# Kernel tuning notes

Measured on AMD Instinct MI355X. Metric: run time of the kernel, lower is better.

Reference implementation:

```python
import jax, jax.numpy as jnp
import numpy as np

NEG_WEIGHT = 0.5   # args_config.lambda_
REG_WEIGHT = 1e-4  # args_config.l2 (dropout rate 0.0 -> identity)

N_USERS, N_ITEMS, DIM = 200000, 1000000, 64
BATCH, HIST = 4096, 200


def setup_inputs() -> dict:
    key = jax.random.key(0)
    k1, k2, k3, k4, k5 = jax.random.split(key, 5)
    users = jax.random.randint(k1, (BATCH,), 0, N_USERS, dtype=jnp.int64 if jax.config.jax_enable_x64 else jnp.int32).astype(jnp.int32)
    hist = jax.random.randint(k2, (N_USERS, HIST), 0, N_ITEMS).astype(jnp.int32)
    user_emb = jax.random.normal(k3, (N_USERS, DIM), dtype=jnp.float32) * 0.1
    item_emb = jax.random.normal(k4, (N_ITEMS, DIM), dtype=jnp.float32) * 0.1
    Hw = jax.random.normal(k5, (1, DIM), dtype=jnp.float32) * 0.1
    return {"users": users, "hist": hist, "user_emb": user_emb,
            "item_emb": item_emb, "Hw": Hw}


def reference(users, hist, user_emb, item_emb, Hw):
    h = Hw[0]                                   # [D]
    u = user_emb[users]                         # [B, D]
    items = item_emb[hist[users]]               # [B, L, D]
    # pos_score[b,l] = sum_d u[b,d] * items[b,l,d] * h[d]  (mul + H_i linear)
    pos_score = jnp.einsum('bd,bld,d->bl', u, items, h)
    # Gram matrices replace bmm(outer).sum(0): E^T E, U_b^T U_b, h h^T
    item_sum = item_emb.T @ item_emb            # [D, D]
    user_sum = u.T @ u                          # [D, D]
    H_sum = jnp.outer(h, h)                     # [D, D]
    t = jnp.sum(item_sum * user_sum * H_sum)
    loss = NEG_WEIGHT * t
    loss = loss + jnp.sum((1.0 - NEG_WEIGHT) * jnp.square(pos_score) - 2.0 * pos_score)
    # reg: 2-norm (Frobenius) of each full embedding table
    reg_loss = REG_WEIGHT * (jnp.linalg.norm(user_emb) + jnp.linalg.norm(item_emb))
    loss = loss + reg_loss
    return (loss, reg_loss, reg_loss)
```

## Files before the change

### kernel.cpp

```cpp
#include <hip/hip_runtime.h>
#include <hip/hip_bf16.h>

typedef __bf16 bf16x8 __attribute__((ext_vector_type(8)));
typedef float f32x16 __attribute__((ext_vector_type(16)));

template<bool GATHER>
static __device__ __forceinline__ void gram_body(
    const float* __restrict__ emb, const int* __restrict__ idx,
    int nrows, int nwaves_total, int blk,
    float* __restrict__ partial, float* __restrict__ red, int t) {
    const int lane = t & 63, wave = t >> 6;
    const int c = lane & 31, kh = lane >> 5;
    const int wid = blk * 4 + wave;
    const int step = nwaves_total * 16;

    f32x16 g00 = {}, g01 = {}, g11 = {};
    float cur0[8], cur1[8];

    int k0 = wid * 16;
    if (k0 < nrows) {
        const int kb = k0 + kh * 8;
#pragma unroll
        for (int j = 0; j < 8; ++j) {
            const size_t rb = (GATHER ? (size_t)idx[kb + j] : (size_t)(kb + j)) * 64;
            cur0[j] = emb[rb + c];
            cur1[j] = emb[rb + 32 + c];
        }
    }
    for (; k0 < nrows; k0 += step) {
        float nx0[8], nx1[8];
        const int k1 = k0 + step;
        if (k1 < nrows) {
            const int kb = k1 + kh * 8;
#pragma unroll
            for (int j = 0; j < 8; ++j) {
                const size_t rb = (GATHER ? (size_t)idx[kb + j] : (size_t)(kb + j)) * 64;
                nx0[j] = emb[rb + c];
                nx1[j] = emb[rb + 32 + c];
            }
        } else {
#pragma unroll
            for (int j = 0; j < 8; ++j) { nx0[j] = 0.f; nx1[j] = 0.f; }
        }
        bf16x8 f0, f1;
#pragma unroll
        for (int j = 0; j < 8; ++j) {
            f0[j] = (__bf16)cur0[j];
            f1[j] = (__bf16)cur1[j];
        }
        g00 = __builtin_amdgcn_mfma_f32_32x32x16_bf16(f0, f0, g00, 0, 0, 0);
        g01 = __builtin_amdgcn_mfma_f32_32x32x16_bf16(f0, f1, g01, 0, 0, 0);
        g11 = __builtin_amdgcn_mfma_f32_32x32x16_bf16(f1, f1, g11, 0, 0, 0);
#pragma unroll
        for (int j = 0; j < 8; ++j) { cur0[j] = nx0[j]; cur1[j] = nx1[j]; }
    }

    __syncthreads();
    for (int w = 0; w < 4; ++w) {
        if (wave == w) {
#pragma unroll
            for (int r = 0; r < 16; ++r) {
                const int cell = ((r & 3) + 8 * (r >> 2) + 4 * kh) * 32 + c;
                if (w == 0) {
                    red[cell] = g00[r]; red[1024 + cell] = g01[r]; red[2048 + cell] = g11[r];
                } else {
                    red[cell] += g00[r]; red[1024 + cell] += g01[r]; red[2048 + cell] += g11[r];
                }
            }
        }
        __syncthreads();
    }
    float* outp = partial + (size_t)blk * 3072;
    for (int i = t; i < 3072; i += 256) outp[i] = red[i];
}

__global__ __launch_bounds__(256) void gram_kernel(
    const float* __restrict__ emb, int nrows, int nwaves_total,
    float* __restrict__ partial) {
    __shared__ float red[3072];
    gram_body<false>(emb, nullptr, nrows, nwaves_total, blockIdx.x,
                     partial, red, threadIdx.x);
}

__global__ __launch_bounds__(256) void mix_kernel(
    const int* __restrict__ users, const int* __restrict__ hist,
    const float* __restrict__ user_emb, const float* __restrict__ item_emb,
    const float* __restrict__ Hw, int batch, int histL, int n_users,
    int NP, int NSS, int NU,
    float* __restrict__ p1, float* __restrict__ p2,
    float* __restrict__ pss, float* __restrict__ partB) {
    __shared__ float red[3072];
    const int bid = blockIdx.x, t = threadIdx.x;

    if (bid < NP) {
        const int lane = t & 63, wave = t >> 6;
        const int w = bid * 4 + wave;
        if (w >= batch) return;
        const int iu = users[w];
        const int k = lane & 15, g = lane >> 4;
        const float4 vu = *reinterpret_cast<const float4*>(user_emb + (size_t)iu * 64 + k * 4);
        const float4 vh = *reinterpret_cast<const float4*>(Hw + k * 4);
        const float4 uh = make_float4(vu.x * vh.x, vu.y * vh.y, vu.z * vh.z, vu.w * vh.w);
        const int* hrow = hist + (size_t)iu * histL;

        float s1 = 0.f, s2 = 0.f;
        int l = g;
        for (; l + 12 < histL; l += 16) {
            int it[4];
#pragma unroll
            for (int u = 0; u < 4; ++u) it[u] = hrow[l + 4 * u];
            float d[4];
#pragma unroll
            for (int u = 0; u < 4; ++u) {
                const float4 v = *reinterpret_cast<const float4*>(
                    item_emb + (size_t)it[u] * 64 + k * 4);
                d[u] = v.x * uh.x + v.y * uh.y + v.z * uh.z + v.w * uh.w;
            }
#pragma unroll
            for (int u = 0; u < 4; ++u) {
                float dd = d[u];
                dd += __shfl_xor(dd, 1, 16);
                dd += __shfl_xor(dd, 2, 16);
                dd += __shfl_xor(dd, 4, 16);
                dd += __shfl_xor(dd, 8, 16);
                s1 += dd;
                s2 = fmaf(dd, dd, s2);
            }
        }
        for (; l < histL; l += 4) {
            const int it = hrow[l];
            const float4 v = *reinterpret_cast<const float4*>(
                item_emb + (size_t)it * 64 + k * 4);
            float dd = v.x * uh.x + v.y * uh.y + v.z * uh.z + v.w * uh.w;
            dd += __shfl_xor(dd, 1, 16);
            dd += __shfl_xor(dd, 2, 16);
            dd += __shfl_xor(dd, 4, 16);
            dd += __shfl_xor(dd, 8, 16);
            s1 += dd;
            s2 = fmaf(dd, dd, s2);
        }
        s1 += __shfl_xor(s1, 16, 64); s1 += __shfl_xor(s1, 32, 64);
        s2 += __shfl_xor(s2, 16, 64); s2 += __shfl_xor(s2, 32, 64);
        if (lane == 0) { p1[w] = s1 * 0.0625f; p2[w] = s2 * 0.0625f; }
    } else if (bid < NP + NSS) {
        const int cid = bid - NP;
        const int n4 = n_users * 16;
        float s = 0.f;
        for (int i = cid * 256 + t; i < n4; i += NSS * 256) {
            const float4 v = reinterpret_cast<const float4*>(user_emb)[i];
            s = fmaf(v.x, v.x, s); s = fmaf(v.y, v.y, s);
            s = fmaf(v.z, v.z, s); s = fmaf(v.w, v.w, s);
        }
#pragma unroll
        for (int off = 32; off >= 1; off >>= 1) s += __shfl_xor(s, off, 64);
        if ((t & 63) == 0) red[t >> 6] = s;
        __syncthreads();
        if (t == 0) pss[cid] = red[0] + red[1] + red[2] + red[3];
    } else {
        gram_body<true>(user_emb, users, batch, NU * 4, bid - NP - NSS,
                        partB, red, t);
    }
}

__global__ __launch_bounds__(256) void reduce_gram_kernel(
    const float* __restrict__ pa, int na,
    const float* __restrict__ pb, int nb, float* __restrict__ part2) {
    const int bid = blockIdx.x;
    const int cellblk = bid % 24, seg = bid / 24;
    const int e = cellblk * 256 + threadIdx.x;
    const float* p; int n, ee;
    if (e < 3072) { p = pa; n = na; ee = e; }
    else          { p = pb; n = nb; ee = e - 3072; }
    const int chunk = (n + 7) >> 3;
    const int b0 = seg * chunk;
    int b1 = b0 + chunk; if (b1 > n) b1 = n;
    float s[4] = {0.f, 0.f, 0.f, 0.f};
    int b = b0;
    for (; b + 4 <= b1; b += 4)
#pragma unroll
        for (int u = 0; u < 4; ++u) s[u] += p[(size_t)(b + u) * 3072 + ee];
    for (; b < b1; ++b) s[0] += p[(size_t)b * 3072 + ee];
    part2[(size_t)seg * 6144 + e] = (s[0] + s[1]) + (s[2] + s[3]);
}

__global__ __launch_bounds__(1024) void finalize_kernel(
    const float* __restrict__ part2, const float* __restrict__ Hw,
    const float* __restrict__ p1, const float* __restrict__ p2, int npos,
    const float* __restrict__ pss, int nss, float* __restrict__ outp) {
    const int t = threadIdx.x;
    float tsum = 0.f, trace = 0.f, s1 = 0.f, s2 = 0.f, su = 0.f;
    for (int e = t; e < 3072; e += 1024) {
        float gi = 0.f, gu = 0.f;
#pragma unroll
        for (int seg = 0; seg < 8; ++seg) {
            gi += part2[(size_t)seg * 6144 + e];
            gu += part2[(size_t)seg * 6144 + 3072 + e];
        }
        const int tile = e >> 10, r = (e & 1023) >> 5, cc = e & 31;
        const int i = (tile == 2) ? r + 32 : r;
        const int j = (tile == 0) ? cc : cc + 32;
        const float w = (tile == 1) ? 2.0f : 1.0f;
        tsum += w * gi * gu * Hw[i] * Hw[j];
        if (i == j) trace += gi;
    }
    for (int e = t; e < npos; e += 1024) { s1 += p1[e]; s2 += p2[e]; }
    for (int e = t; e < nss; e += 1024) su += pss[e];
#pragma unroll
    for (int off = 32; off >= 1; off >>= 1) {
        tsum += __shfl_xor(tsum, off, 64);
        trace += __shfl_xor(trace, off, 64);
        s1 += __shfl_xor(s1, off, 64);
        s2 += __shfl_xor(s2, off, 64);
        su += __shfl_xor(su, off, 64);
    }
    __shared__ float rr[16][5];
    if ((t & 63) == 0) {
        const int w = t >> 6;
        rr[w][0] = tsum; rr[w][1] = trace; rr[w][2] = s1;
        rr[w][3] = s2;   rr[w][4] = su;
    }
    __syncthreads();
    if (t == 0) {
        float a[5] = {0.f, 0.f, 0.f, 0.f, 0.f};
        for (int w = 0; w < 16; ++w)
#pragma unroll
            for (int q = 0; q < 5; ++q) a[q] += rr[w][q];
        const float reg = 1e-4f * (sqrtf(a[4]) + sqrtf(a[1]));
        const float loss = 0.5f * a[0] + 0.5f * a[3] - 2.0f * a[2] + reg;
        outp[0] = loss; outp[1] = reg; outp[2] = reg;
    }
}

extern "C" void kernel_launch(void* const* d_in, const int* in_sizes, int n_in,
                              void* d_out, int out_size, void* d_ws, size_t ws_size,
                              hipStream_t stream) {
    const int*   users    = (const int*)d_in[0];
    const int*   hist     = (const int*)d_in[1];
    const float* user_emb = (const float*)d_in[2];
    const float* item_emb = (const float*)d_in[3];
    const float* Hw       = (const float*)d_in[4];
    float* outp = (float*)d_out;
    float* ws   = (float*)d_ws;

    const int n_users = in_sizes[2] / 64;
    const int n_items = in_sizes[3] / 64;
    const int batch   = in_sizes[0];
    const int histL   = in_sizes[1] / n_users;

    int NB_ITEM = 1024;
    const int NP  = (batch + 3) / 4;
    const int NSS = 512;
    const int NU  = 64;

    const size_t o_p1 = 0;
    const size_t o_p2 = o_p1 + (size_t)batch;
    const size_t o_ss = o_p2 + (size_t)batch;
    const size_t o_part2 = o_ss + NSS;
    const size_t o_part = o_part2 + 8 * 6144;
    long availf = (long)(ws_size / 4) - (long)o_part - (long)NU * 3072;
    if ((long)NB_ITEM * 3072 > availf) {
        NB_ITEM = (int)(availf / 3072);
        if (NB_ITEM < 8) NB_ITEM = 8;
    }
    float* partA = ws + o_part;
    float* partB = partA + (size_t)NB_ITEM * 3072;

    gram_kernel<<<NB_ITEM, 256, 0, stream>>>(
        item_emb, n_items, NB_ITEM * 4, partA);
    mix_kernel<<<NP + NSS + NU, 256, 0, stream>>>(
        users, hist, user_emb, item_emb, Hw, batch, histL, n_users,
        NP, NSS, NU, ws + o_p1, ws + o_p2, ws + o_ss, partB);
    reduce_gram_kernel<<<24 * 8, 256, 0, stream>>>(
        partA, NB_ITEM, partB, NU, ws + o_part2);
    finalize_kernel<<<1, 1024, 0, stream>>>(
        ws + o_part2, Hw, ws + o_p1, ws + o_p2, batch,
        ws + o_ss, NSS, outp);
}
```

Before: 111.7 us.

## Fuse item Gram kernel into mixed kernel and rebalance block counts

Merges the separate item-embedding Gram kernel into the mixed kernel, so the item Gram, the positive-score gather, the user sum-of-squares and the user Gram all run as block ranges of one launch and can overlap on the GPU. The positive-score section becomes a grid-stride loop over users with a fixed 512 blocks, and the block counts are retuned (768 item-Gram blocks, 192 sum-of-squares blocks, launch bounds with 6 blocks per CU). This removes one launch and the tail gap between the first two kernels, at the cost of coarser load balance and possible register pressure from the new launch bound.

```diff
diff --git a/kernel.cpp b/kernel.cpp
--- a/kernel.cpp
+++ b/kernel.cpp
@@ -74,51 +74,60 @@
     for (int i = t; i < 3072; i += 256) outp[i] = red[i];
 }
 
-__global__ __launch_bounds__(256) void gram_kernel(
-    const float* __restrict__ emb, int nrows, int nwaves_total,
-    float* __restrict__ partial) {
-    __shared__ float red[3072];
-    gram_body<false>(emb, nullptr, nrows, nwaves_total, blockIdx.x,
-                     partial, red, threadIdx.x);
-}
-
-__global__ __launch_bounds__(256) void mix_kernel(
+__global__ __launch_bounds__(256, 6) void fused_kernel(
     const int* __restrict__ users, const int* __restrict__ hist,
     const float* __restrict__ user_emb, const float* __restrict__ item_emb,
-    const float* __restrict__ Hw, int batch, int histL, int n_users,
-    int NP, int NSS, int NU,
-    float* __restrict__ p1, float* __restrict__ p2,
-    float* __restrict__ pss, float* __restrict__ partB) {
+    const float* __restrict__ Hw,
+    int n_users, int n_items, int batch, int histL,
+    int NA, int NP, int NSS, int NU,
+    float* __restrict__ partA, float* __restrict__ partB,
+    float* __restrict__ p1, float* __restrict__ p2, float* __restrict__ pss) {
     __shared__ float red[3072];
     const int bid = blockIdx.x, t = threadIdx.x;
 
-    if (bid < NP) {
+    if (bid < NA) {
+        gram_body<false>(item_emb, nullptr, n_items, NA * 4, bid,
+                         partA, red, t);
+    } else if (bid < NA + NP) {
+        const int pid = bid - NA;
         const int lane = t & 63, wave = t >> 6;
-        const int w = bid * 4 + wave;
-        if (w >= batch) return;
-        const int iu = users[w];
         const int k = lane & 15, g = lane >> 4;
-        const float4 vu = *reinterpret_cast<const float4*>(user_emb + (size_t)iu * 64 + k * 4);
-        const float4 vh = *reinterpret_cast<const float4*>(Hw + k * 4);
-        const float4 uh = make_float4(vu.x * vh.x, vu.y * vh.y, vu.z * vh.z, vu.w * vh.w);
-        const int* hrow = hist + (size_t)iu * histL;
-
-        float s1 = 0.f, s2 = 0.f;
-        int l = g;
-        for (; l + 12 < histL; l += 16) {
-            int it[4];
-#pragma unroll
-            for (int u = 0; u < 4; ++u) it[u] = hrow[l + 4 * u];
-            float d[4];
-#pragma unroll
-            for (int u = 0; u < 4; ++u) {
+        for (int w = pid * 4 + wave; w < batch; w += NP * 4) {
+            const int iu = users[w];
+            const float4 vu = *reinterpret_cast<const float4*>(user_emb + (size_t)iu * 64 + k * 4);
+            const float4 vh = *reinterpret_cast<const float4*>(Hw + k * 4);
+            const float4 uh = make_float4(vu.x * vh.x, vu.y * vh.y, vu.z * vh.z, vu.w * vh.w);
+            const int* hrow = hist + (size_t)iu * histL;
+
+            float s1 = 0.f, s2 = 0.f;
+            int l = g;
+            for (; l + 12 < histL; l += 16) {
+                int it[4];
+#pragma unroll
+                for (int u = 0; u < 4; ++u) it[u] = hrow[l + 4 * u];
+                float d[4];
+#pragma unroll
+                for (int u = 0; u < 4; ++u) {
+                    const float4 v = *reinterpret_cast<const float4*>(
+                        item_emb + (size_t)it[u] * 64 + k * 4);
+                    d[u] = v.x * uh.x + v.y * uh.y + v.z * uh.z + v.w * uh.w;
+                }
+#pragma unroll
+                for (int u = 0; u < 4; ++u) {
+                    float dd = d[u];
+                    dd += __shfl_xor(dd, 1, 16);
+                    dd += __shfl_xor(dd, 2, 16);
+                    dd += __shfl_xor(dd, 4, 16);
+                    dd += __shfl_xor(dd, 8, 16);
+                    s1 += dd;
+                    s2 = fmaf(dd, dd, s2);
+                }
+            }
+            for (; l < histL; l += 4) {
+                const int it = hrow[l];
                 const float4 v = *reinterpret_cast<const float4*>(
-                    item_emb + (size_t)it[u] * 64 + k * 4);
-                d[u] = v.x * uh.x + v.y * uh.y + v.z * uh.z + v.w * uh.w;
-            }
-#pragma unroll
-            for (int u = 0; u < 4; ++u) {
-                float dd = d[u];
+                    item_emb + (size_t)it * 64 + k * 4);
+                float dd = v.x * uh.x + v.y * uh.y + v.z * uh.z + v.w * uh.w;
                 dd += __shfl_xor(dd, 1, 16);
                 dd += __shfl_xor(dd, 2, 16);
                 dd += __shfl_xor(dd, 4, 16);
@@ -126,24 +135,12 @@
                 s1 += dd;
                 s2 = fmaf(dd, dd, s2);
             }
-        }
-        for (; l < histL; l += 4) {
-            const int it = hrow[l];
-            const float4 v = *reinterpret_cast<const float4*>(
-                item_emb + (size_t)it * 64 + k * 4);
-            float dd = v.x * uh.x + v.y * uh.y + v.z * uh.z + v.w * uh.w;
-            dd += __shfl_xor(dd, 1, 16);
-            dd += __shfl_xor(dd, 2, 16);
-            dd += __shfl_xor(dd, 4, 16);
-            dd += __shfl_xor(dd, 8, 16);
-            s1 += dd;
-            s2 = fmaf(dd, dd, s2);
-        }
-        s1 += __shfl_xor(s1, 16, 64); s1 += __shfl_xor(s1, 32, 64);
-        s2 += __shfl_xor(s2, 16, 64); s2 += __shfl_xor(s2, 32, 64);
-        if (lane == 0) { p1[w] = s1 * 0.0625f; p2[w] = s2 * 0.0625f; }
-    } else if (bid < NP + NSS) {
-        const int cid = bid - NP;
+            s1 += __shfl_xor(s1, 16, 64); s1 += __shfl_xor(s1, 32, 64);
+            s2 += __shfl_xor(s2, 16, 64); s2 += __shfl_xor(s2, 32, 64);
+            if (lane == 0) { p1[w] = s1 * 0.0625f; p2[w] = s2 * 0.0625f; }
+        }
+    } else if (bid < NA + NP + NSS) {
+        const int cid = bid - NA - NP;
         const int n4 = n_users * 16;
         float s = 0.f;
         for (int i = cid * 256 + t; i < n4; i += NSS * 256) {
@@ -157,7 +154,7 @@
         __syncthreads();
         if (t == 0) pss[cid] = red[0] + red[1] + red[2] + red[3];
     } else {
-        gram_body<true>(user_emb, users, batch, NU * 4, bid - NP - NSS,
+        gram_body<true>(user_emb, users, batch, NU * 4, bid - NA - NP - NSS,
                         partB, red, t);
     }
 }
@@ -247,9 +244,9 @@
     const int batch   = in_sizes[0];
     const int histL   = in_sizes[1] / n_users;
 
-    int NB_ITEM = 1024;
-    const int NP  = (batch + 3) / 4;
-    const int NSS = 512;
+    int NA = 768;
+    const int NP  = 512;
+    const int NSS = 192;
     const int NU  = 64;
 
     const size_t o_p1 = 0;
@@ -258,20 +255,20 @@
     const size_t o_part2 = o_ss + NSS;
     const size_t o_part = o_part2 + 8 * 6144;
     long availf = (long)(ws_size / 4) - (long)o_part - (long)NU * 3072;
-    if ((long)NB_ITEM * 3072 > availf) {
-        NB_ITEM = (int)(availf / 3072);
-        if (NB_ITEM < 8) NB_ITEM = 8;
+    if ((long)NA * 3072 > availf) {
+        NA = (int)(availf / 3072);
+        if (NA < 8) NA = 8;
     }
     float* partA = ws + o_part;
-    float* partB = partA + (size_t)NB_ITEM * 3072;
-
-    gram_kernel<<<NB_ITEM, 256, 0, stream>>>(
-        item_emb, n_items, NB_ITEM * 4, partA);
-    mix_kernel<<<NP + NSS + NU, 256, 0, stream>>>(
-        users, hist, user_emb, item_emb, Hw, batch, histL, n_users,
-        NP, NSS, NU, ws + o_p1, ws + o_p2, ws + o_ss, partB);
+    float* partB = partA + (size_t)NA * 3072;
+
+    fused_kernel<<<NA + NP + NSS + NU, 256, 0, stream>>>(
+        users, hist, user_emb, item_emb, Hw,
+        n_users, n_items, batch, histL,
+        NA, NP, NSS, NU,
+        partA, partB, ws + o_p1, ws + o_p2, ws + o_ss);
     reduce_gram_kernel<<<24 * 8, 256, 0, stream>>>(
-        partA, NB_ITEM, partB, NU, ws + o_part2);
+        partA, NA, partB, NU, ws + o_part2);
     finalize_kernel<<<1, 1024, 0, stream>>>(
         ws + o_part2, Hw, ws + o_p1, ws + o_p2, batch,
         ws + o_ss, NSS, outp);
```

Result: slower. 119.4 us (+6.9%).
